# Optimization experiments

Hardware: AMD Instinct MI355X
Metric: run time of the kernel (lower is better)

Reference implementation:

```python
import jax, jax.numpy as jnp
import numpy as np

M = 8
EPS = 1e-5


def _bn(x, gamma, beta):
    # x: [T, N, C]; torch BatchNorm1d on [T, C, N] (training mode) normalizes
    # over batch and length dims -> axes (0, 1) here, biased variance.
    mean = jnp.mean(x, axis=(0, 1))
    var = jnp.var(x, axis=(0, 1))
    return (x - mean) * jax.lax.rsqrt(var + EPS) * gamma + beta


def setup_inputs() -> dict:
    key = jax.random.key(0)
    T, N, E = 128, 256, 128
    ks = jax.random.split(key, 16)
    s = 1.0 / np.sqrt(E)
    inp = {
        "node": jax.random.normal(ks[0], (T, N, E), dtype=jnp.float32),
        "Wq": jax.random.uniform(ks[1], (E, E), jnp.float32, -s, s),
        "bq": jax.random.uniform(ks[2], (E,), jnp.float32, -s, s),
        "Wk": jax.random.uniform(ks[3], (E, E), jnp.float32, -s, s),
        "bk": jax.random.uniform(ks[4], (E,), jnp.float32, -s, s),
        "Wv": jax.random.uniform(ks[5], (E, E), jnp.float32, -s, s),
        "bv": jax.random.uniform(ks[6], (E,), jnp.float32, -s, s),
        "Ww": jax.random.uniform(ks[7], (E, E), jnp.float32, -s, s),
        "bw": jax.random.uniform(ks[8], (E,), jnp.float32, -s, s),
        "Wf1": jax.random.uniform(ks[9], (4 * E, E), jnp.float32, -s, s),
        "bf1": jax.random.uniform(ks[10], (4 * E,), jnp.float32, -s, s),
        "Wf2": jax.random.uniform(ks[11], (E, 4 * E), jnp.float32, -0.5 * s, 0.5 * s),
        "bf2": jax.random.uniform(ks[12], (E,), jnp.float32, -0.5 * s, 0.5 * s),
        "g1": jnp.ones((E,), jnp.float32),
        "be1": jnp.zeros((E,), jnp.float32),
        "g2": jnp.ones((E,), jnp.float32),
        "be2": jnp.zeros((E,), jnp.float32),
        "temp_len": T,
    }
    return inp


def reference(node, Wq, bq, Wk, bk, Wv, bv, Ww, bw, Wf1, bf1, Wf2, bf2,
              g1, be1, g2, be2, temp_len):
    T, N, E = node.shape
    D = E // M          # head dim = 16
    dk = E / M          # softmax scale denominator (embedding_size / M)

    q = (node @ Wq.T + bq).reshape(T, N, M, D)
    k = (node @ Wk.T + bk).reshape(T, N, M, D)
    v = (node @ Wv.T + bv).reshape(T, N, M, D)

    # scores[t,n,j,m] = sum_d q[t,n,m,d]*k[t,j,m,d] / sqrt(dk)
    scores = jnp.einsum('tnmd,tjmd->tnjm', q, k) / jnp.sqrt(jnp.float32(dk))
    attn = jax.nn.softmax(scores, axis=2)  # softmax over key dim (dim=2)

    # out[t,n,m,d] = sum_j attn[t,n,j,m] * v[t,j,m,d]
    out = jnp.einsum('tnjm,tjmd->tnmd', attn, v).reshape(T, N, E)

    x = out @ Ww.T + bw + node
    x = _bn(x, g1, be1)

    x1 = jax.nn.relu(x @ Wf1.T + bf1) @ Wf2.T + bf2
    x = x + x1
    x = _bn(x, g2, be2)
    return x
```

## Files before the change

### kernel.cpp

```cpp
#include <hip/hip_runtime.h>
#include <stdint.h>

typedef unsigned int  uint32;
typedef unsigned short u16;
typedef __attribute__((ext_vector_type(8))) short short8;
typedef __attribute__((ext_vector_type(4))) float f32x4;
typedef __attribute__((ext_vector_type(4))) _Float16 half4;

__device__ __forceinline__ float bits2f(uint32 u){ union{uint32 u; float f;} c; c.u=u; return c.f; }
__device__ __forceinline__ uint32 f2bits(float f){ union{uint32 u; float f;} c; c.f=f; return c.u; }
__device__ __forceinline__ u16 f2b(float f){ uint32 u=f2bits(f); return (u16)((u + 0x7FFFu + ((u>>16)&1u))>>16); }
__device__ __forceinline__ float b2f(u16 h){ return bits2f(((uint32)h)<<16); }
__device__ __forceinline__ u16 f2h(float f){ _Float16 h=(_Float16)f; union{u16 u; _Float16 h;} c; c.h=h; return c.u; }
__device__ __forceinline__ float4 ld4f(const float* p){ return *(const float4*)p; }
#define BLO(u) bits2f((u)<<16)
#define BHI(u) bits2f((u)&0xFFFF0000u)

#define QKS 24

__device__ __forceinline__ void load_ab(const float* __restrict__ gacc,
                                        const float* __restrict__ gam,
                                        const float* __restrict__ bet,
                                        float* sA, float* sB, int t)
{
  if (t < 128) {
    const float mean = gacc[t] * (1.f/32768.f);
    const float var  = gacc[128 + t] * (1.f/32768.f) - mean * mean;
    const float rstd = rsqrtf(var + 1e-5f);
    const float Ac = gam[t] * rstd;
    sA[t] = Ac;
    sB[t] = bet[t] - mean * Ac;
  }
  __syncthreads();
}

template<int OMODE, int RES, bool RELU, bool AF32, bool WF32, bool BNA, bool STATS, int JT>
__device__ __forceinline__ void gemm_tile(
    u16* As, u16* Ws, const float* sA, const float* sB, float* pS, float* pQ,
    const void* Ain, const void* W, const float* bias, const void* res,
    float* gacc_out, void* out, int row0, int col0, int K, int Nout,
    float oscale, int t)
{
  constexpr int WROWS = JT * 32;
  const int L = t & 63, w = t >> 6;
  const int wrow = (w >> 1) * 64, wcol = (w & 1) * (JT * 16);
  const int lm = L & 15, lg = L >> 4;

  f32x4 acc[4][JT];
#pragma unroll
  for (int i = 0; i < 4; ++i)
#pragma unroll
    for (int j = 0; j < JT; ++j) acc[i][j] = (f32x4){0.f,0.f,0.f,0.f};

  const int srow = t >> 1, skc = (t & 1) * 32;
  const u16*   Ab = (const u16*)Ain + (size_t)(row0 + srow) * K + skc;
  const float* Af = (const float*)Ain + (size_t)(row0 + srow) * K + skc;
  u16* Asp = As + srow * 72 + skc;
  constexpr int TPR = 256 / WROWS;
  const int wsrow = t / TPR, wskc = (t % TPR) * (64 / TPR);
  const u16*   Wp  = (const u16*)W + (size_t)(col0 + wsrow) * K + wskc;
  const float* Wpf = (const float*)W + (size_t)(col0 + wsrow) * K + wskc;
  u16* Wsp = Ws + wsrow * 72 + wskc;
  constexpr int NW = (64 / TPR) / 8;

  short8 ga[4]; short8 gw[NW];
  float4 fa[4][2]; float4 fw[NW][2];

  auto load_chunk = [&](int k0) {
    if constexpr (AF32) {
#pragma unroll
      for (int i = 0; i < 4; ++i) {
        fa[i][0] = ld4f(Af + k0 + i*8);
        fa[i][1] = ld4f(Af + k0 + i*8 + 4);
      }
    } else {
#pragma unroll
      for (int i = 0; i < 4; ++i) ga[i] = *(const short8*)(Ab + k0 + i*8);
    }
    if constexpr (WF32) {
#pragma unroll
      for (int i = 0; i < NW; ++i) {
        fw[i][0] = ld4f(Wpf + k0 + i*8);
        fw[i][1] = ld4f(Wpf + k0 + i*8 + 4);
      }
    } else {
#pragma unroll
      for (int i = 0; i < NW; ++i) gw[i] = *(const short8*)(Wp + k0 + i*8);
    }
  };

  auto write_chunk = [&](int k0) {
    if constexpr (AF32) {
#pragma unroll
      for (int i = 0; i < 4; ++i) {
        short8 s;
        s[0]=(short)f2b(fa[i][0].x); s[1]=(short)f2b(fa[i][0].y);
        s[2]=(short)f2b(fa[i][0].z); s[3]=(short)f2b(fa[i][0].w);
        s[4]=(short)f2b(fa[i][1].x); s[5]=(short)f2b(fa[i][1].y);
        s[6]=(short)f2b(fa[i][1].z); s[7]=(short)f2b(fa[i][1].w);
        *(short8*)(Asp + i*8) = s;
      }
    } else if constexpr (BNA) {
#pragma unroll
      for (int i = 0; i < 4; ++i) {
        const int c = skc + k0 + i*8;
        const short8 x8 = ga[i];
        const float4 A0 = *(const float4*)&sA[c], A1 = *(const float4*)&sA[c+4];
        const float4 B0 = *(const float4*)&sB[c], B1 = *(const float4*)&sB[c+4];
        short8 s;
        s[0]=(short)f2b(b2f((u16)x8[0])*A0.x+B0.x); s[1]=(short)f2b(b2f((u16)x8[1])*A0.y+B0.y);
        s[2]=(short)f2b(b2f((u16)x8[2])*A0.z+B0.z); s[3]=(short)f2b(b2f((u16)x8[3])*A0.w+B0.w);
        s[4]=(short)f2b(b2f((u16)x8[4])*A1.x+B1.x); s[5]=(short)f2b(b2f((u16)x8[5])*A1.y+B1.y);
        s[6]=(short)f2b(b2f((u16)x8[6])*A1.z+B1.z); s[7]=(short)f2b(b2f((u16)x8[7])*A1.w+B1.w);
        *(short8*)(Asp + i*8) = s;
      }
    } else {
#pragma unroll
      for (int i = 0; i < 4; ++i) *(short8*)(Asp + i*8) = ga[i];
    }
    if constexpr (WF32) {
#pragma unroll
      for (int i = 0; i < NW; ++i) {
        short8 s;
        s[0]=(short)f2b(fw[i][0].x); s[1]=(short)f2b(fw[i][0].y);
        s[2]=(short)f2b(fw[i][0].z); s[3]=(short)f2b(fw[i][0].w);
        s[4]=(short)f2b(fw[i][1].x); s[5]=(short)f2b(fw[i][1].y);
        s[6]=(short)f2b(fw[i][1].z); s[7]=(short)f2b(fw[i][1].w);
        *(short8*)(Wsp + i*8) = s;
      }
    } else {
#pragma unroll
      for (int i = 0; i < NW; ++i) *(short8*)(Wsp + i*8) = gw[i];
    }
  };

  load_chunk(0);
  for (int k0 = 0; k0 < K; k0 += 64) {
    __syncthreads();
    write_chunk(k0);
    __syncthreads();
    if (k0 + 64 < K) load_chunk(k0 + 64);
#pragma unroll
    for (int ks = 0; ks < 64; ks += 32) {
      short8 af[4], wf[JT];
#pragma unroll
      for (int i = 0; i < 4; ++i)
        af[i] = *(const short8*)(As + (wrow + i*16 + lm) * 72 + ks + lg*8);
#pragma unroll
      for (int j = 0; j < JT; ++j)
        wf[j] = *(const short8*)(Ws + (wcol + j*16 + lm) * 72 + ks + lg*8);
#pragma unroll
      for (int i = 0; i < 4; ++i)
#pragma unroll
        for (int j = 0; j < JT; ++j)
          acc[i][j] = __builtin_amdgcn_mfma_f32_16x16x32_bf16(af[i], wf[j], acc[i][j], 0, 0, 0);
    }
  }

  float bj[JT];
#pragma unroll
  for (int j = 0; j < JT; ++j) bj[j] = bias[col0 + wcol + j*16 + lm];

  float stS[JT], stQ[JT];
#pragma unroll
  for (int j = 0; j < JT; ++j) { stS[j] = 0.f; stQ[j] = 0.f; }

#pragma unroll
  for (int i = 0; i < 4; ++i) {
    const int rowb = row0 + wrow + i*16 + lg*4;
#pragma unroll
    for (int j = 0; j < JT; ++j) {
      const int col = col0 + wcol + j*16 + lm;
      float ra = 0.f, rb = 0.f;
      if constexpr (RES == 3) { ra = sA[col & 127]; rb = sB[col & 127]; }
      if constexpr (OMODE == 3) {
        const int tt = rowb >> 8, n0 = rowb & 255;
        const int mh = col >> 4, d = col & 15;
        uint2 o;
        o.x = (uint32)f2h(acc[i][j][0] + bj[j]) | ((uint32)f2h(acc[i][j][1] + bj[j]) << 16);
        o.y = (uint32)f2h(acc[i][j][2] + bj[j]) | ((uint32)f2h(acc[i][j][3] + bj[j]) << 16);
        *(uint2*)((u16*)out + (((size_t)tt*8 + mh)*16 + d)*256 + n0) = o;
      } else {
#pragma unroll
        for (int r = 0; r < 4; ++r) {
          const int row = rowb + r;
          float v = acc[i][j][r] + bj[j];
          if constexpr (RES == 1) v += ((const float*)res)[(size_t)row*128 + col];
          if constexpr (RES == 3) v += b2f(((const u16*)res)[(size_t)row*128 + col]) * ra + rb;
          if constexpr (RELU) v = fmaxf(v, 0.f);
          if constexpr (STATS) { stS[j] += v; stQ[j] += v*v; }
          if constexpr (OMODE == 2) {
            const int tt = row >> 8, n = row & 255, mh = col >> 4, d = col & 15;
            ((u16*)out)[(((size_t)tt*8 + mh)*256 + n)*16 + d] = f2h(v * oscale);
          } else {
            ((u16*)out)[(size_t)row * Nout + col] = f2b(v);
          }
        }
      }
    }
  }

  if constexpr (STATS) {
    __syncthreads();
    if (t < 128) { pS[t] = 0.f; pQ[t] = 0.f; }
    __syncthreads();
#pragma unroll
    for (int j = 0; j < JT; ++j) {
      const int col = col0 + wcol + j*16 + lm;
      atomicAdd(&pS[col], stS[j]);
      atomicAdd(&pQ[col], stQ[j]);
    }
    __syncthreads();
    if (t < 128) {
      atomicAdd(&gacc_out[t],       pS[t]);
      atomicAdd(&gacc_out[128 + t], pQ[t]);
    }
  }
}

__global__ __launch_bounds__(256)
void qkv_k(const float* __restrict__ node,
           const float* __restrict__ Wq, const float* __restrict__ bq,
           const float* __restrict__ Wk, const float* __restrict__ bk,
           const float* __restrict__ Wv, const float* __restrict__ bv,
           const float* __restrict__ Ww, const float* __restrict__ Wf1,
           const float* __restrict__ Wf2,
           u16* __restrict__ qb, u16* __restrict__ kb, u16* __restrict__ vb,
           u16* __restrict__ wb, float* __restrict__ accbuf)
{
  const int bid = blockIdx.x, t = threadIdx.x;
  if (bid < 768) {
    __shared__ u16 As[128*72];
    __shared__ u16 Ws[128*72];
    __shared__ __align__(16) float sA[128], sB[128];
    __shared__ float pS[128], pQ[128];
    const int x = bid & 255, y = bid >> 8;
    const float QSCALE = 0.36067376022224085f;
    if (y == 0)
      gemm_tile<2,0,false,true,true,false,false,4>(As,Ws,sA,sB,pS,pQ, node, Wq, bq,
          nullptr, nullptr, qb, x*128, 0, 128, 128, QSCALE, t);
    else if (y == 1)
      gemm_tile<2,0,false,true,true,false,false,4>(As,Ws,sA,sB,pS,pQ, node, Wk, bk,
          nullptr, nullptr, kb, x*128, 0, 128, 128, 1.f, t);
    else
      gemm_tile<3,0,false,true,true,false,false,4>(As,Ws,sA,sB,pS,pQ, node, Wv, bv,
          nullptr, nullptr, vb, x*128, 0, 128, 128, 1.f, t);
  } else if (bid < 912) {
    const int i = (bid - 768) * 256 + t;
    const float4* src; u16* dst;
    if      (i <  4096) { src = (const float4*)Ww  + i;         dst = wb +  49152 + (size_t)i*4; }
    else if (i < 20480) { src = (const float4*)Wf1 + (i-4096);  dst = wb +  65536 + (size_t)(i-4096)*4; }
    else                { src = (const float4*)Wf2 + (i-20480); dst = wb + 131072 + (size_t)(i-20480)*4; }
    float4 v = *src;
    uint2 o;
    o.x = (uint32)f2b(v.x) | ((uint32)f2b(v.y) << 16);
    o.y = (uint32)f2b(v.z) | ((uint32)f2b(v.w) << 16);
    *(uint2*)dst = o;
  } else {
    accbuf[t] = 0.f;
    accbuf[256 + t] = 0.f;
  }
}

__global__ __launch_bounds__(256)
void oproj_k(const u16* __restrict__ ab, const u16* __restrict__ wwb,
             const float* __restrict__ bw, const float* __restrict__ node,
             float* __restrict__ accbuf, u16* __restrict__ xb)
{
  __shared__ u16 As[128*72];
  __shared__ u16 Ws[64*72];
  __shared__ __align__(16) float sA[128], sB[128];
  __shared__ float pS[128], pQ[128];
  gemm_tile<0,1,false,false,false,false,true,2>(As,Ws,sA,sB,pS,pQ, ab, wwb, bw,
      node, accbuf, xb, blockIdx.x*128, blockIdx.y*64, 128, 128, 1.f, threadIdx.x);
}

#define HS_LD 520
#define AS_LD 136
#define WS_LD 72

__global__ __launch_bounds__(512)
void ffn_k(const u16* __restrict__ xb, const u16* __restrict__ wf1b,
           const float* __restrict__ bf1, const u16* __restrict__ wf2b,
           const float* __restrict__ bf2, const float* __restrict__ accbuf,
           const float* __restrict__ g1, const float* __restrict__ be1,
           float* __restrict__ acc2, u16* __restrict__ x2b)
{
  __shared__ u16 Hs[64*HS_LD];
  __shared__ u16 As[64*AS_LD];
  __shared__ u16 Ws[128*WS_LD];
  __shared__ __align__(16) float sA[128], sB[128];
  __shared__ float pS[128], pQ[128];

  const int t = threadIdx.x;
  const int row0 = blockIdx.x * 64;
  load_ab(accbuf, g1, be1, sA, sB, t);

  {
    const int r = t >> 3, seg = (t & 7) * 16;
    const u16* src = xb + (size_t)(row0 + r) * 128 + seg;
    u16* dst = As + r * AS_LD + seg;
#pragma unroll
    for (int h = 0; h < 2; ++h) {
      const short8 x8 = *(const short8*)(src + h*8);
      const int c = seg + h*8;
      const float4 A0 = *(const float4*)&sA[c], A1 = *(const float4*)&sA[c+4];
      const float4 B0 = *(const float4*)&sB[c], B1 = *(const float4*)&sB[c+4];
      short8 s;
      s[0]=(short)f2b(b2f((u16)x8[0])*A0.x+B0.x); s[1]=(short)f2b(b2f((u16)x8[1])*A0.y+B0.y);
      s[2]=(short)f2b(b2f((u16)x8[2])*A0.z+B0.z); s[3]=(short)f2b(b2f((u16)x8[3])*A0.w+B0.w);
      s[4]=(short)f2b(b2f((u16)x8[4])*A1.x+B1.x); s[5]=(short)f2b(b2f((u16)x8[5])*A1.y+B1.y);
      s[6]=(short)f2b(b2f((u16)x8[6])*A1.z+B1.z); s[7]=(short)f2b(b2f((u16)x8[7])*A1.w+B1.w);
      *(short8*)(dst + h*8) = s;
    }
  }

  const int w = t >> 6, L = t & 63, lm = L & 15, lg = L >> 4;
  const int wcol = w * 16;
  const int wr = t >> 2, kc = (t & 3) * 16;

  auto wsrc = [&](int cc) -> const u16* {
    if (cc < 8) return wf1b + (size_t)((cc>>1)*128 + wr)*128 + (cc&1)*64 + kc;
    return wf2b + (size_t)wr*512 + (cc-8)*64 + kc;
  };

  f32x4 accF[4];
#pragma unroll
  for (int i = 0; i < 4; ++i) accF[i] = (f32x4){0.f,0.f,0.f,0.f};

  short8 gw0 = *(const short8*)(wsrc(0));
  short8 gw1 = *(const short8*)(wsrc(0) + 8);

  for (int cc = 0; cc < 16; ++cc) {
    __syncthreads();
    *(short8*)(Ws + wr*WS_LD + kc)     = gw0;
    *(short8*)(Ws + wr*WS_LD + kc + 8) = gw1;
    __syncthreads();
    if (cc < 15) {
      gw0 = *(const short8*)(wsrc(cc+1));
      gw1 = *(const short8*)(wsrc(cc+1) + 8);
    }
    const u16* Abase = (cc < 8) ? (As + ((size_t)(cc & 1) * 64))
                                : (Hs + ((size_t)(cc - 8) * 64));
    const int ald = (cc < 8) ? AS_LD : HS_LD;
#pragma unroll
    for (int ks = 0; ks < 64; ks += 32) {
      short8 af[4], wf;
#pragma unroll
      for (int i = 0; i < 4; ++i)
        af[i] = *(const short8*)(Abase + (i*16 + lm) * ald + ks + lg*8);
      wf = *(const short8*)(Ws + (wcol + lm) * WS_LD + ks + lg*8);
#pragma unroll
      for (int i = 0; i < 4; ++i)
        accF[i] = __builtin_amdgcn_mfma_f32_16x16x32_bf16(af[i], wf, accF[i], 0, 0, 0);
    }
    if (cc < 8 && (cc & 1)) {
      const int ct = cc >> 1;
      const float b1 = bf1[ct*128 + wcol + lm];
#pragma unroll
      for (int i = 0; i < 4; ++i) {
#pragma unroll
        for (int r = 0; r < 4; ++r) {
          const int row = i*16 + lg*4 + r;
          Hs[row*HS_LD + ct*128 + wcol + lm] = f2b(fmaxf(accF[i][r] + b1, 0.f));
        }
        accF[i] = (f32x4){0.f,0.f,0.f,0.f};
      }
    }
  }

  const int col = wcol + lm;
  const float b2 = bf2[col];
  const float ra = sA[col], rb = sB[col];
  float stS = 0.f, stQ = 0.f;
#pragma unroll
  for (int i = 0; i < 4; ++i) {
#pragma unroll
    for (int r = 0; r < 4; ++r) {
      const int row = row0 + i*16 + lg*4 + r;
      float v = accF[i][r] + b2 + b2f(xb[(size_t)row*128 + col]) * ra + rb;
      stS += v; stQ += v*v;
      x2b[(size_t)row*128 + col] = f2b(v);
    }
  }
  __syncthreads();
  if (t < 128) { pS[t] = 0.f; pQ[t] = 0.f; }
  __syncthreads();
  atomicAdd(&pS[col], stS);
  atomicAdd(&pQ[col], stQ);
  __syncthreads();
  if (t < 128) {
    atomicAdd(&acc2[t],       pS[t]);
    atomicAdd(&acc2[128 + t], pQ[t]);
  }
}

__global__ __launch_bounds__(256)
void attn_k(const u16* __restrict__ q, const u16* __restrict__ k,
            const u16* __restrict__ v, u16* __restrict__ ab)
{
  __shared__ __align__(16) u16 Qs[256*QKS];
  __shared__ __align__(16) u16 Ks[256*QKS];
  __shared__ __align__(16) u16 Vt[16*264];
  const int tm = blockIdx.x, tt = tm >> 3, m = tm & 7;
  const int t = threadIdx.x;

  const uint4* qg = (const uint4*)(q + (size_t)tm*4096);
  const uint4* kg = (const uint4*)(k + (size_t)tm*4096);
  const uint4* vg = (const uint4*)(v + (size_t)tm*4096);
#pragma unroll
  for (int p = t; p < 512; p += 256) {
    const uint4 a = qg[p], b = kg[p], c = vg[p];
    const int row = p >> 1, h = (p & 1) * 8;
    *(uint4*)(Qs + row*QKS + h) = a;
    *(uint4*)(Ks + row*QKS + h) = b;
    *(uint4*)(Vt + (p >> 5)*264 + (p & 31)*8) = c;
  }
  __syncthreads();

  const int w = t >> 6, L = t & 63, lm = L & 15, quad = L >> 4;

  half4 vf[16];
#pragma unroll
  for (int jt = 0; jt < 16; ++jt)
    vf[jt] = *(const half4*)(Vt + lm*264 + jt*16 + quad*4);

  for (int nt = 0; nt < 4; ++nt) {
    const half4 bq = *(const half4*)(Qs + ((w*4 + nt)*16 + lm)*QKS + quad*4);
    f32x4 s[16];
#pragma unroll
    for (int jt = 0; jt < 16; ++jt) {
      const half4 af = *(const half4*)(Ks + (jt*16 + lm)*QKS + quad*4);
      s[jt] = __builtin_amdgcn_mfma_f32_16x16x16f16(af, bq, (f32x4){0.f,0.f,0.f,0.f}, 0, 0, 0);
    }
    float mx = s[0][0];
#pragma unroll
    for (int jt = 0; jt < 16; ++jt)
#pragma unroll
      for (int r = 0; r < 4; ++r) mx = fmaxf(mx, s[jt][r]);
    mx = fmaxf(mx, __shfl_xor(mx, 16));
    mx = fmaxf(mx, __shfl_xor(mx, 32));
    float ls = 0.f;
#pragma unroll
    for (int jt = 0; jt < 16; ++jt)
#pragma unroll
      for (int r = 0; r < 4; ++r) { const float p = exp2f(s[jt][r] - mx); s[jt][r] = p; ls += p; }
    ls += __shfl_xor(ls, 16);
    ls += __shfl_xor(ls, 32);

    f32x4 oacc = {0.f,0.f,0.f,0.f};
#pragma unroll
    for (int jt = 0; jt < 16; ++jt) {
      half4 pf;
      pf[0] = (_Float16)s[jt][0]; pf[1] = (_Float16)s[jt][1];
      pf[2] = (_Float16)s[jt][2]; pf[3] = (_Float16)s[jt][3];
      oacc = __builtin_amdgcn_mfma_f32_16x16x16f16(pf, vf[jt], oacc, 0, 0, 0);
    }
    const int q0 = w*64 + nt*16 + quad*4;
#pragma unroll
    for (int r = 0; r < 4; ++r) {
      const float lr = __shfl(ls, quad*4 + r);
      ab[((size_t)tt*256 + q0 + r)*128 + m*16 + lm] = f2b(oacc[r] / lr);
    }
  }
}

__global__ __launch_bounds__(256)
void bn_final(const uint2* __restrict__ x2, const float* __restrict__ gacc,
              const float* __restrict__ gam, const float* __restrict__ bet,
              float* __restrict__ out)
{
  __shared__ __align__(16) float sA[128], sB[128];
  const int t = threadIdx.x;
  load_ab(gacc, gam, bet, sA, sB, t);
#pragma unroll 2
  for (int kk = 0; kk < 8; ++kk) {
    const size_t idx = (size_t)blockIdx.x * 2048 + kk * 256 + t;
    const uint2 u = x2[idx];
    const int c = (int)((idx & 31) * 4);
    const f32x4 A = *(const f32x4*)&sA[c];
    const f32x4 B = *(const f32x4*)&sB[c];
    f32x4 o;
    o[0] = BLO(u.x)*A[0] + B[0];
    o[1] = BHI(u.x)*A[1] + B[1];
    o[2] = BLO(u.y)*A[2] + B[2];
    o[3] = BHI(u.y)*A[3] + B[3];
    *(f32x4*)(out + idx*4) = o;
  }
}

extern "C" void kernel_launch(void* const* d_in, const int* in_sizes, int n_in,
                              void* d_out, int out_size, void* d_ws, size_t ws_size,
                              hipStream_t stream)
{
  (void)in_sizes; (void)n_in; (void)out_size; (void)ws_size;
  const float* node = (const float*)d_in[0];
  const float* Wq  = (const float*)d_in[1];  const float* bq  = (const float*)d_in[2];
  const float* Wk  = (const float*)d_in[3];  const float* bk  = (const float*)d_in[4];
  const float* Wv  = (const float*)d_in[5];  const float* bv  = (const float*)d_in[6];
  const float* Ww  = (const float*)d_in[7];  const float* bw  = (const float*)d_in[8];
  const float* Wf1 = (const float*)d_in[9];  const float* bf1 = (const float*)d_in[10];
  const float* Wf2 = (const float*)d_in[11]; const float* bf2 = (const float*)d_in[12];
  const float* g1  = (const float*)d_in[13]; const float* be1 = (const float*)d_in[14];
  const float* g2  = (const float*)d_in[15]; const float* be2 = (const float*)d_in[16];
  float* out = (float*)d_out;
  char* ws = (char*)d_ws;

  u16* wb  = (u16*)(ws + 0);
  u16* qb  = (u16*)(ws + 524288);
  u16* kb  = (u16*)(ws + 8912896);
  u16* vb  = (u16*)(ws + 17301504);
  u16* ab  = (u16*)(ws + 25690112);
  u16* xb  = (u16*)(ws + 34078720);
  u16* x2b = (u16*)(ws + 42467328);
  float* accbuf = (float*)(ws + 50855936);

  u16* wwb = wb + 49152;  u16* wf1b = wb + 65536; u16* wf2b = wb + 131072;

  dim3 blk(256);

  qkv_k<<<dim3(913), blk, 0, stream>>>(node, Wq,bq, Wk,bk, Wv,bv, Ww, Wf1, Wf2,
                                       qb, kb, vb, wb, accbuf);
  attn_k<<<dim3(1024), blk, 0, stream>>>(qb, kb, vb, ab);
  oproj_k<<<dim3(256,2), blk, 0, stream>>>(ab, wwb, bw, node, accbuf, xb);
  ffn_k<<<dim3(512), dim3(512), 0, stream>>>(xb, wf1b, bf1, wf2b, bf2,
                                             accbuf, g1, be1, accbuf + 256, x2b);
  bn_final<<<dim3(512), blk, 0, stream>>>((const uint2*)x2b, accbuf + 256, g2, be2, out);
}
```

Baseline: 210.7 us.

## Split FFN hidden dimension into two halves to halve hidden LDS buffer

The FFN kernel now processes the 512-wide hidden layer in two halves of 256: it computes half of the first GEMM, immediately consumes it in the second GEMM into a separate accumulator, then repeats. This halves the shared-memory hidden buffer (stride 264 instead of 520), so more blocks can be resident per CU, and launch bounds request 4 blocks. The cost is an extra set of accumulator registers and a tighter register budget under the new launch bound, which could cause spills.

```diff
diff --git a/kernel.cpp b/kernel.cpp
--- a/kernel.cpp
+++ b/kernel.cpp
@@ -275,18 +275,18 @@
       node, accbuf, xb, blockIdx.x*128, blockIdx.y*64, 128, 128, 1.f, threadIdx.x);
 }
 
-#define HS_LD 520
+#define HS2_LD 264
 #define AS_LD 136
 #define WS_LD 72
 
-__global__ __launch_bounds__(512)
+__global__ __launch_bounds__(512, 4)
 void ffn_k(const u16* __restrict__ xb, const u16* __restrict__ wf1b,
            const float* __restrict__ bf1, const u16* __restrict__ wf2b,
            const float* __restrict__ bf2, const float* __restrict__ accbuf,
            const float* __restrict__ g1, const float* __restrict__ be1,
            float* __restrict__ acc2, u16* __restrict__ x2b)
 {
-  __shared__ u16 Hs[64*HS_LD];
+  __shared__ u16 Hs[64*HS2_LD];
   __shared__ u16 As[64*AS_LD];
   __shared__ u16 Ws[128*WS_LD];
   __shared__ __align__(16) float sA[128], sB[128];
@@ -319,30 +319,37 @@
   const int wcol = w * 16;
   const int wr = t >> 2, kc = (t & 3) * 16;
 
-  auto wsrc = [&](int cc) -> const u16* {
-    if (cc < 8) return wf1b + (size_t)((cc>>1)*128 + wr)*128 + (cc&1)*64 + kc;
-    return wf2b + (size_t)wr*512 + (cc-8)*64 + kc;
+  auto wsrc = [&](int g) -> const u16* {
+    const int half = g >> 3, cc = g & 7;
+    if (cc < 4) return wf1b + (size_t)((2*half + (cc>>1))*128 + wr)*128 + (cc&1)*64 + kc;
+    return wf2b + (size_t)wr*512 + half*256 + (cc-4)*64 + kc;
   };
 
   f32x4 accF[4];
-#pragma unroll
-  for (int i = 0; i < 4; ++i) accF[i] = (f32x4){0.f,0.f,0.f,0.f};
+  f32x4 acc2r[4];
+#pragma unroll
+  for (int i = 0; i < 4; ++i) {
+    accF[i]  = (f32x4){0.f,0.f,0.f,0.f};
+    acc2r[i] = (f32x4){0.f,0.f,0.f,0.f};
+  }
 
   short8 gw0 = *(const short8*)(wsrc(0));
   short8 gw1 = *(const short8*)(wsrc(0) + 8);
 
-  for (int cc = 0; cc < 16; ++cc) {
+  for (int g = 0; g < 16; ++g) {
+    const int cc = g & 7;
+    const bool is1 = (cc < 4);
     __syncthreads();
     *(short8*)(Ws + wr*WS_LD + kc)     = gw0;
     *(short8*)(Ws + wr*WS_LD + kc + 8) = gw1;
     __syncthreads();
-    if (cc < 15) {
-      gw0 = *(const short8*)(wsrc(cc+1));
-      gw1 = *(const short8*)(wsrc(cc+1) + 8);
-    }
-    const u16* Abase = (cc < 8) ? (As + ((size_t)(cc & 1) * 64))
-                                : (Hs + ((size_t)(cc - 8) * 64));
-    const int ald = (cc < 8) ? AS_LD : HS_LD;
+    if (g < 15) {
+      gw0 = *(const short8*)(wsrc(g+1));
+      gw1 = *(const short8*)(wsrc(g+1) + 8);
+    }
+    const u16* Abase = is1 ? (As + ((size_t)(cc & 1) * 64))
+                           : (Hs + ((size_t)(cc - 4) * 64));
+    const int ald = is1 ? AS_LD : HS2_LD;
 #pragma unroll
     for (int ks = 0; ks < 64; ks += 32) {
       short8 af[4], wf;
@@ -350,19 +357,27 @@
       for (int i = 0; i < 4; ++i)
         af[i] = *(const short8*)(Abase + (i*16 + lm) * ald + ks + lg*8);
       wf = *(const short8*)(Ws + (wcol + lm) * WS_LD + ks + lg*8);
-#pragma unroll
-      for (int i = 0; i < 4; ++i)
-        accF[i] = __builtin_amdgcn_mfma_f32_16x16x32_bf16(af[i], wf, accF[i], 0, 0, 0);
-    }
-    if (cc < 8 && (cc & 1)) {
-      const int ct = cc >> 1;
+      if (is1) {
+#pragma unroll
+        for (int i = 0; i < 4; ++i)
+          accF[i] = __builtin_amdgcn_mfma_f32_16x16x32_bf16(af[i], wf, accF[i], 0, 0, 0);
+      } else {
+#pragma unroll
+        for (int i = 0; i < 4; ++i)
+          acc2r[i] = __builtin_amdgcn_mfma_f32_16x16x32_bf16(af[i], wf, acc2r[i], 0, 0, 0);
+      }
+    }
+    if (is1 && (cc & 1)) {
+      const int half = g >> 3;
+      const int ct = 2*half + (cc >> 1);
+      const int lct = cc >> 1;
       const float b1 = bf1[ct*128 + wcol + lm];
 #pragma unroll
       for (int i = 0; i < 4; ++i) {
 #pragma unroll
         for (int r = 0; r < 4; ++r) {
           const int row = i*16 + lg*4 + r;
-          Hs[row*HS_LD + ct*128 + wcol + lm] = f2b(fmaxf(accF[i][r] + b1, 0.f));
+          Hs[row*HS2_LD + lct*128 + wcol + lm] = f2b(fmaxf(accF[i][r] + b1, 0.f));
         }
         accF[i] = (f32x4){0.f,0.f,0.f,0.f};
       }
@@ -378,7 +393,7 @@
 #pragma unroll
     for (int r = 0; r < 4; ++r) {
       const int row = row0 + i*16 + lg*4 + r;
-      float v = accF[i][r] + b2 + b2f(xb[(size_t)row*128 + col]) * ra + rb;
+      float v = acc2r[i][r] + b2 + b2f(xb[(size_t)row*128 + col]) * ra + rb;
       stS += v; stQ += v*v;
       x2b[(size_t)row*128 + col] = f2b(v);
     }
```

Result: faster. 200.4 us (-4.9%).
